# Optimization experiments

Hardware: AMD Instinct MI355X
Metric: run time of the kernel (lower is better)

The kernel has to match this reference:

```python
import jax, jax.numpy as jnp
import numpy as np

NEG_SLOPE = 0.2


def _gat_conv(x, src, dst, W, a_l, a_r, b, n_nodes, activate):
    """DGL-style GATConv. x:[N,F_in], W:[F_in,H*D], a_l/a_r/b:[H,D]."""
    H, D = a_l.shape
    feat = (x @ W).reshape(n_nodes, H, D)                      # [N,H,D]
    el = jnp.sum(feat * a_l, axis=-1)                          # [N,H]
    er = jnp.sum(feat * a_r, axis=-1)                          # [N,H]
    e = jax.nn.leaky_relu(el[src] + er[dst], NEG_SLOPE)        # [E,H]
    # edge softmax over incoming edges of each dst node (numerically stable)
    emax = jax.ops.segment_max(e, dst, num_segments=n_nodes)   # [N,H]
    emax = jnp.where(jnp.isfinite(emax), emax, 0.0)            # zero-in-degree safe
    ee = jnp.exp(e - emax[dst])                                # [E,H]
    denom = jax.ops.segment_sum(ee, dst, num_segments=n_nodes) # [N,H]
    alpha = ee / jnp.maximum(denom[dst], 1e-9)                 # [E,H]
    # aggregate alpha-weighted src features into dst
    msg = alpha[:, :, None] * feat[src]                        # [E,H,D]
    out = jax.ops.segment_sum(msg, dst, num_segments=n_nodes)  # [N,H,D]
    out = out + b
    if activate:
        out = jax.nn.elu(out)
    return out


def setup_inputs() -> dict:
    key = jax.random.key(0)
    ks = jax.random.split(key, 16)
    N, E, F_in, H, Dh, C = 50000, 800000, 256, 4, 64, 40
    s = lambda fan_in: 1.0 / np.sqrt(fan_in)
    return {
        "x": jax.random.normal(ks[0], (N, F_in), dtype=jnp.float32),
        "edge_index": jax.random.randint(ks[1], (2, E), 0, N, dtype=jnp.int32),
        "W0": jax.random.normal(ks[2], (F_in, H * Dh), dtype=jnp.float32) * s(F_in),
        "al0": jax.random.normal(ks[3], (H, Dh), dtype=jnp.float32) * s(Dh),
        "ar0": jax.random.normal(ks[4], (H, Dh), dtype=jnp.float32) * s(Dh),
        "b0": jnp.zeros((H, Dh), dtype=jnp.float32),
        "W1": jax.random.normal(ks[5], (H * Dh, H * Dh), dtype=jnp.float32) * s(H * Dh),
        "al1": jax.random.normal(ks[6], (H, Dh), dtype=jnp.float32) * s(Dh),
        "ar1": jax.random.normal(ks[7], (H, Dh), dtype=jnp.float32) * s(Dh),
        "b1": jnp.zeros((H, Dh), dtype=jnp.float32),
        "W2": jax.random.normal(ks[8], (H * Dh, H * C), dtype=jnp.float32) * s(H * Dh),
        "al2": jax.random.normal(ks[9], (H, C), dtype=jnp.float32) * s(C),
        "ar2": jax.random.normal(ks[10], (H, C), dtype=jnp.float32) * s(C),
        "b2": jnp.zeros((H, C), dtype=jnp.float32),
    }


def reference(x, edge_index, W0, al0, ar0, b0, W1, al1, ar1, b1, W2, al2, ar2, b2):
    N = x.shape[0]
    src, dst = edge_index[0], edge_index[1]
    h = _gat_conv(x, src, dst, W0, al0, ar0, b0, N, activate=True).reshape(N, -1)
    h = _gat_conv(h, src, dst, W1, al1, ar1, b1, N, activate=True).reshape(N, -1)
    out = _gat_conv(h, src, dst, W2, al2, ar2, b2, N, activate=False)
    logits = out.mean(axis=1)  # mean over heads -> [N, num_classes]
    return logits
```

## Files before the change

### kernel.cpp

```cpp
#include <hip/hip_runtime.h>
#include <hip/hip_bf16.h>
#include <math.h>

#define NEG_SLOPE 0.2f

typedef unsigned short ushortT;
typedef __attribute__((ext_vector_type(8))) short short8;
typedef __attribute__((ext_vector_type(4))) float f32x4;

static __device__ __forceinline__ float leaky(float x){ return x > 0.f ? x : NEG_SLOPE * x; }
static __device__ __forceinline__ float elu(float x){ return x > 0.f ? x : (__expf(x) - 1.f); }

static __device__ __forceinline__ ushortT f2bf(float f){
  unsigned u = __float_as_uint(f);
  u += 0x7fff + ((u >> 16) & 1);
  return (ushortT)(u >> 16);
}
static __device__ __forceinline__ float bf2f(ushortT h){ return __uint_as_float((unsigned)h << 16); }
static __device__ __forceinline__ float bf_lo(unsigned u){ return __uint_as_float(u << 16); }
static __device__ __forceinline__ float bf_hi(unsigned u){ return __uint_as_float(u & 0xffff0000u); }

__global__ void hist_kernel(const int* __restrict__ dst, int E, int* __restrict__ counts){
  int i = blockIdx.x*blockDim.x + threadIdx.x;
  if(i < E) atomicAdd(&counts[dst[i]], 1);
}

__global__ void scan1_kernel(const int* __restrict__ counts, int N,
                             int* __restrict__ offsets, int* __restrict__ blocksums){
  __shared__ int sdata[1024];
  int i = blockIdx.x*1024 + threadIdx.x;
  int v = (i<N) ? counts[i] : 0;
  sdata[threadIdx.x] = v;
  __syncthreads();
  for(int off=1; off<1024; off<<=1){
    int t = (threadIdx.x >= off) ? sdata[threadIdx.x-off] : 0;
    __syncthreads();
    sdata[threadIdx.x] += t;
    __syncthreads();
  }
  if(i<N) offsets[i] = sdata[threadIdx.x] - v;
  if(threadIdx.x==1023) blocksums[blockIdx.x] = sdata[1023];
}

__global__ void scan2_kernel(int* __restrict__ blocksums, int nb){
  __shared__ int sdata[64];
  int v = ((int)threadIdx.x < nb) ? blocksums[threadIdx.x] : 0;
  sdata[threadIdx.x] = v;
  __syncthreads();
  for(int off=1; off<64; off<<=1){
    int t = (threadIdx.x >= off) ? sdata[threadIdx.x-off] : 0;
    __syncthreads();
    sdata[threadIdx.x] += t;
    __syncthreads();
  }
  if((int)threadIdx.x < nb) blocksums[threadIdx.x] = sdata[threadIdx.x] - v;
}

__global__ void scan3_kernel(int* __restrict__ offsets, const int* __restrict__ blocksums,
                             int N, int E, int* __restrict__ cursor){
  int i = blockIdx.x*1024 + threadIdx.x;
  if(i < N){
    int o = offsets[i] + blocksums[blockIdx.x];
    offsets[i] = o;
    cursor[i] = o;
  }
  if(i == 0) offsets[N] = E;
}

__global__ void scatter_kernel(const int* __restrict__ src, const int* __restrict__ dst, int E,
                               int* __restrict__ cursor, int* __restrict__ ssrc,
                               int* __restrict__ sdst){
  int i = blockIdx.x*blockDim.x + threadIdx.x;
  if(i < E){
    int d = dst[i];
    int p = atomicAdd(&cursor[d], 1);
    ssrc[p] = src[i];
    sdst[p] = d;
  }
}

__global__ __launch_bounds__(256) void wsplit_kernel(const float* __restrict__ W, int N,
                              ushortT* __restrict__ Wth, ushortT* __restrict__ Wtl){
  int idx = blockIdx.x*256 + threadIdx.x;
  int n = idx >> 8, k = idx & 255;
  float v = (n < N) ? W[(size_t)k*N + n] : 0.f;
  ushortT h = f2bf(v);
  ushortT l = f2bf(v - bf2f(h));
  Wth[idx] = h; Wtl[idx] = l;
}

#define GBM 128
#define GBN 128
#define GBK 32
#define LSTR 40
__global__ __launch_bounds__(256) void gemm_mfma(const float* __restrict__ A,
                       const ushortT* __restrict__ Bth, const ushortT* __restrict__ Btl,
                       ushortT* __restrict__ Cm, int M, int N, int K){
  __shared__ ushortT Ah[GBM*LSTR], Al[GBM*LSTR], Bh[GBN*LSTR], Bl[GBN*LSTR];
  const int tid  = threadIdx.x;
  const int lane = tid & 63;
  const int wv   = tid >> 6;
  const int wr   = wv >> 1, wc = wv & 1;
  const int m0   = blockIdx.y * GBM;
  const int n0   = blockIdx.x * GBN;
  const int l15  = lane & 15, quad = lane >> 4;

  f32x4 acc[4][4];
  #pragma unroll
  for(int i=0;i<4;i++)
    #pragma unroll
    for(int j=0;j<4;j++){ acc[i][j][0]=0.f; acc[i][j][1]=0.f; acc[i][j][2]=0.f; acc[i][j][3]=0.f; }

  for(int k0=0; k0<K; k0+=GBK){
    #pragma unroll
    for(int i=0;i<4;i++){
      int r  = (tid>>3) + i*32;
      int cq = (tid&7)*4;
      float4 v = make_float4(0.f,0.f,0.f,0.f);
      int gm = m0 + r;
      if(gm < M) v = *(const float4*)&A[(size_t)gm*K + k0 + cq];
      ushortT h0=f2bf(v.x), h1=f2bf(v.y), h2=f2bf(v.z), h3=f2bf(v.w);
      ushort4 hv = make_ushort4(h0,h1,h2,h3);
      ushort4 lv = make_ushort4(f2bf(v.x-bf2f(h0)), f2bf(v.y-bf2f(h1)),
                                f2bf(v.z-bf2f(h2)), f2bf(v.w-bf2f(h3)));
      *(ushort4*)&Ah[r*LSTR + cq] = hv;
      *(ushort4*)&Al[r*LSTR + cq] = lv;
    }
    {
      int n  = tid >> 1;
      int kh = (tid & 1) * 16;
      const ushortT* bhrow = &Bth[(size_t)(n0+n)*K + k0 + kh];
      const ushortT* blrow = &Btl[(size_t)(n0+n)*K + k0 + kh];
      uint4 hv0 = *(const uint4*)(bhrow);
      uint4 hv1 = *(const uint4*)(bhrow + 8);
      uint4 lv0 = *(const uint4*)(blrow);
      uint4 lv1 = *(const uint4*)(blrow + 8);
      *(uint4*)&Bh[n*LSTR + kh]     = hv0;
      *(uint4*)&Bh[n*LSTR + kh + 8] = hv1;
      *(uint4*)&Bl[n*LSTR + kh]     = lv0;
      *(uint4*)&Bl[n*LSTR + kh + 8] = lv1;
    }
    __syncthreads();
    short8 a_h[4], a_l[4], b_h[4], b_l[4];
    #pragma unroll
    for(int i=0;i<4;i++){
      int m = wr*64 + i*16 + l15;
      a_h[i] = *(short8*)&Ah[m*LSTR + quad*8];
      a_l[i] = *(short8*)&Al[m*LSTR + quad*8];
    }
    #pragma unroll
    for(int j=0;j<4;j++){
      int n = wc*64 + j*16 + l15;
      b_h[j] = *(short8*)&Bh[n*LSTR + quad*8];
      b_l[j] = *(short8*)&Bl[n*LSTR + quad*8];
    }
    #pragma unroll
    for(int i=0;i<4;i++)
      #pragma unroll
      for(int j=0;j<4;j++){
        acc[i][j] = __builtin_amdgcn_mfma_f32_16x16x32_bf16(a_h[i], b_h[j], acc[i][j], 0,0,0);
        acc[i][j] = __builtin_amdgcn_mfma_f32_16x16x32_bf16(a_h[i], b_l[j], acc[i][j], 0,0,0);
        acc[i][j] = __builtin_amdgcn_mfma_f32_16x16x32_bf16(a_l[i], b_h[j], acc[i][j], 0,0,0);
      }
    __syncthreads();
  }
  #pragma unroll
  for(int i=0;i<4;i++){
    #pragma unroll
    for(int r=0;r<4;r++){
      int gm = m0 + wr*64 + i*16 + quad*4 + r;
      if(gm >= M) continue;
      #pragma unroll
      for(int j=0;j<4;j++){
        int gn = n0 + wc*64 + j*16 + l15;
        if(gn < N) Cm[(size_t)gm*N + gn] = f2bf(acc[i][j][r]);
      }
    }
  }
}

__global__ void attn_proj_bf(const __hip_bfloat16* __restrict__ feat, const float* __restrict__ a_l,
                             const float* __restrict__ a_r, float* __restrict__ el,
                             float* __restrict__ er, int D){
  int n = blockIdx.x;
  int h = threadIdx.x >> 6;
  int lane = threadIdx.x & 63;
  float vl = 0.f, vr = 0.f;
  for(int d=lane; d<D; d+=64){
    float f = (float)feat[(size_t)n*4*D + h*D + d];
    vl = fmaf(f, a_l[h*D+d], vl);
    vr = fmaf(f, a_r[h*D+d], vr);
  }
  #pragma unroll
  for(int off=32; off; off>>=1){ vl += __shfl_down(vl,off); vr += __shfl_down(vr,off); }
  if(lane==0){ el[n*4+h] = vl; er[n*4+h] = vr; }
}

__global__ __launch_bounds__(256) void edge_w_kernel(const int* __restrict__ ssrc,
                              const int* __restrict__ sdst, int E,
                              const float4* __restrict__ el4, const float4* __restrict__ er4,
                              float4* __restrict__ ew){
  int e = blockIdx.x*blockDim.x + threadIdx.x;
  if(e >= E) return;
  int s = ssrc[e], d = sdst[e];
  float4 l = el4[s], r = er4[d];
  float4 w;
  w.x = __expf(leaky(l.x + r.x));
  w.y = __expf(leaky(l.y + r.y));
  w.z = __expf(leaky(l.z + r.z));
  w.w = __expf(leaky(l.w + r.w));
  ew[e] = w;
}

__global__ __launch_bounds__(256) void agg_kernel(const uint2* __restrict__ feat2,
                           const float* __restrict__ ew,
                           const int* __restrict__ offsets, const int* __restrict__ ssrc,
                           const float* __restrict__ bias, float* __restrict__ outp, int N){
  int wv = threadIdx.x >> 6;
  int lane = threadIdx.x & 63;
  int n = blockIdx.x*4 + wv;
  if(n >= N) return;
  int h = lane >> 4;
  int e0 = offsets[n], e1 = offsets[n+1];
  float4 acc0 = make_float4(0.f,0.f,0.f,0.f), acc1 = acc0, acc2 = acc0, acc3 = acc0;
  float den0 = 0.f, den1 = 0.f, den2 = 0.f, den3 = 0.f;
  int e = e0;
  for(; e+3 < e1; e += 4){
    int s0 = ssrc[e], s1 = ssrc[e+1], s2 = ssrc[e+2], s3 = ssrc[e+3];
    float w0 = ew[(size_t)e*4 + h];
    float w1 = ew[(size_t)(e+1)*4 + h];
    float w2 = ew[(size_t)(e+2)*4 + h];
    float w3 = ew[(size_t)(e+3)*4 + h];
    uint2 q0 = feat2[(size_t)s0*64 + lane];
    uint2 q1 = feat2[(size_t)s1*64 + lane];
    uint2 q2 = feat2[(size_t)s2*64 + lane];
    uint2 q3 = feat2[(size_t)s3*64 + lane];
    acc0.x = fmaf(w0,bf_lo(q0.x),acc0.x); acc0.y = fmaf(w0,bf_hi(q0.x),acc0.y);
    acc0.z = fmaf(w0,bf_lo(q0.y),acc0.z); acc0.w = fmaf(w0,bf_hi(q0.y),acc0.w); den0 += w0;
    acc1.x = fmaf(w1,bf_lo(q1.x),acc1.x); acc1.y = fmaf(w1,bf_hi(q1.x),acc1.y);
    acc1.z = fmaf(w1,bf_lo(q1.y),acc1.z); acc1.w = fmaf(w1,bf_hi(q1.y),acc1.w); den1 += w1;
    acc2.x = fmaf(w2,bf_lo(q2.x),acc2.x); acc2.y = fmaf(w2,bf_hi(q2.x),acc2.y);
    acc2.z = fmaf(w2,bf_lo(q2.y),acc2.z); acc2.w = fmaf(w2,bf_hi(q2.y),acc2.w); den2 += w2;
    acc3.x = fmaf(w3,bf_lo(q3.x),acc3.x); acc3.y = fmaf(w3,bf_hi(q3.x),acc3.y);
    acc3.z = fmaf(w3,bf_lo(q3.y),acc3.z); acc3.w = fmaf(w3,bf_hi(q3.y),acc3.w); den3 += w3;
  }
  for(; e < e1; e++){
    int s = ssrc[e];
    float w = ew[(size_t)e*4 + h];
    uint2 q = feat2[(size_t)s*64 + lane];
    acc0.x = fmaf(w,bf_lo(q.x),acc0.x); acc0.y = fmaf(w,bf_hi(q.x),acc0.y);
    acc0.z = fmaf(w,bf_lo(q.y),acc0.z); acc0.w = fmaf(w,bf_hi(q.y),acc0.w); den0 += w;
  }
  float denom = (den0+den1) + (den2+den3);
  float4 acc;
  acc.x = (acc0.x+acc1.x) + (acc2.x+acc3.x);
  acc.y = (acc0.y+acc1.y) + (acc2.y+acc3.y);
  acc.z = (acc0.z+acc1.z) + (acc2.z+acc3.z);
  acc.w = (acc0.w+acc1.w) + (acc2.w+acc3.w);
  float inv = 1.f / fmaxf(denom, 1e-9f);
  float4 b4 = *(const float4*)&bias[lane*4];
  float4 o;
  o.x = elu(acc.x*inv + b4.x);
  o.y = elu(acc.y*inv + b4.y);
  o.z = elu(acc.z*inv + b4.z);
  o.w = elu(acc.w*inv + b4.w);
  *(float4*)&outp[(size_t)n*256 + lane*4] = o;
}

__global__ __launch_bounds__(256) void agg2_kernel(const uint2* __restrict__ feat2,
                            const float* __restrict__ ew,
                            const int* __restrict__ offsets, const int* __restrict__ ssrc,
                            const float* __restrict__ bias, float* __restrict__ logits, int N){
  __shared__ float s_out[4][160];
  int wv = threadIdx.x >> 6;
  int lane = threadIdx.x & 63;
  int n = blockIdx.x*4 + wv;
  bool valid = (n < N);
  if(valid && lane < 40){
    int h = lane / 10;
    int e0 = offsets[n], e1 = offsets[n+1];
    float4 acc0 = make_float4(0.f,0.f,0.f,0.f), acc1 = acc0, acc2 = acc0, acc3 = acc0;
    float den0 = 0.f, den1 = 0.f, den2 = 0.f, den3 = 0.f;
    int e = e0;
    for(; e+3 < e1; e += 4){
      int s0 = ssrc[e], s1 = ssrc[e+1], s2 = ssrc[e+2], s3 = ssrc[e+3];
      float w0 = ew[(size_t)e*4 + h];
      float w1 = ew[(size_t)(e+1)*4 + h];
      float w2 = ew[(size_t)(e+2)*4 + h];
      float w3 = ew[(size_t)(e+3)*4 + h];
      uint2 q0 = feat2[(size_t)s0*40 + lane];
      uint2 q1 = feat2[(size_t)s1*40 + lane];
      uint2 q2 = feat2[(size_t)s2*40 + lane];
      uint2 q3 = feat2[(size_t)s3*40 + lane];
      acc0.x = fmaf(w0,bf_lo(q0.x),acc0.x); acc0.y = fmaf(w0,bf_hi(q0.x),acc0.y);
      acc0.z = fmaf(w0,bf_lo(q0.y),acc0.z); acc0.w = fmaf(w0,bf_hi(q0.y),acc0.w); den0 += w0;
      acc1.x = fmaf(w1,bf_lo(q1.x),acc1.x); acc1.y = fmaf(w1,bf_hi(q1.x),acc1.y);
      acc1.z = fmaf(w1,bf_lo(q1.y),acc1.z); acc1.w = fmaf(w1,bf_hi(q1.y),acc1.w); den1 += w1;
      acc2.x = fmaf(w2,bf_lo(q2.x),acc2.x); acc2.y = fmaf(w2,bf_hi(q2.x),acc2.y);
      acc2.z = fmaf(w2,bf_lo(q2.y),acc2.z); acc2.w = fmaf(w2,bf_hi(q2.y),acc2.w); den2 += w2;
      acc3.x = fmaf(w3,bf_lo(q3.x),acc3.x); acc3.y = fmaf(w3,bf_hi(q3.x),acc3.y);
      acc3.z = fmaf(w3,bf_lo(q3.y),acc3.z); acc3.w = fmaf(w3,bf_hi(q3.y),acc3.w); den3 += w3;
    }
    for(; e < e1; e++){
      int s = ssrc[e];
      float w = ew[(size_t)e*4 + h];
      uint2 q = feat2[(size_t)s*40 + lane];
      acc0.x = fmaf(w,bf_lo(q.x),acc0.x); acc0.y = fmaf(w,bf_hi(q.x),acc0.y);
      acc0.z = fmaf(w,bf_lo(q.y),acc0.z); acc0.w = fmaf(w,bf_hi(q.y),acc0.w); den0 += w;
    }
    float denom = (den0+den1) + (den2+den3);
    float4 acc;
    acc.x = (acc0.x+acc1.x) + (acc2.x+acc3.x);
    acc.y = (acc0.y+acc1.y) + (acc2.y+acc3.y);
    acc.z = (acc0.z+acc1.z) + (acc2.z+acc3.z);
    acc.w = (acc0.w+acc1.w) + (acc2.w+acc3.w);
    float inv = 1.f / fmaxf(denom, 1e-9f);
    float4 b4 = *(const float4*)&bias[lane*4];
    s_out[wv][lane*4+0] = acc.x*inv + b4.x;
    s_out[wv][lane*4+1] = acc.y*inv + b4.y;
    s_out[wv][lane*4+2] = acc.z*inv + b4.z;
    s_out[wv][lane*4+3] = acc.w*inv + b4.w;
  }
  __syncthreads();
  if(valid && lane < 40){
    logits[(size_t)n*40 + lane] =
        0.25f * (s_out[wv][lane] + s_out[wv][40+lane] + s_out[wv][80+lane] + s_out[wv][120+lane]);
  }
}

extern "C" void kernel_launch(void* const* d_in, const int* in_sizes, int n_in,
                              void* d_out, int out_size, void* d_ws, size_t ws_size,
                              hipStream_t stream){
  const float* x   = (const float*)d_in[0];
  const int*   eix = (const int*)  d_in[1];
  const float* W0  = (const float*)d_in[2];
  const float* al0 = (const float*)d_in[3];
  const float* ar0 = (const float*)d_in[4];
  const float* b0  = (const float*)d_in[5];
  const float* W1  = (const float*)d_in[6];
  const float* al1 = (const float*)d_in[7];
  const float* ar1 = (const float*)d_in[8];
  const float* b1  = (const float*)d_in[9];
  const float* W2  = (const float*)d_in[10];
  const float* al2 = (const float*)d_in[11];
  const float* ar2 = (const float*)d_in[12];
  const float* b2  = (const float*)d_in[13];
  float* logits = (float*)d_out;

  const int N = in_sizes[0] / 256;
  const int E = in_sizes[1] / 2;
  const int* src = eix;
  const int* dst = eix + E;
  const int nb = (N + 1023) / 1024;

  char* ws = (char*)d_ws;
  auto alloc = [&](size_t bytes)->char*{
    char* p = ws; ws += (bytes + 255) & ~(size_t)255; return p;
  };
  int*   counts    = (int*)  alloc((size_t)N*4);
  int*   offsets   = (int*)  alloc((size_t)(N+1)*4);
  int*   cursor    = (int*)  alloc((size_t)N*4);
  int*   blocksums = (int*)  alloc((size_t)nb*4);
  int*   ssrc      = (int*)  alloc((size_t)E*4);
  int*   sdst      = (int*)  alloc((size_t)E*4);
  float* ew        = (float*)alloc((size_t)E*4*4);
  __hip_bfloat16* bufF = (__hip_bfloat16*)alloc((size_t)N*256*2);
  float* bufH      = (float*)alloc((size_t)N*256*4);
  float* el_buf    = (float*)alloc((size_t)N*4*4);
  float* er_buf    = (float*)alloc((size_t)N*4*4);
  ushortT* Wth0 = (ushortT*)alloc(256*256*2);
  ushortT* Wtl0 = (ushortT*)alloc(256*256*2);
  ushortT* Wth1 = (ushortT*)alloc(256*256*2);
  ushortT* Wtl1 = (ushortT*)alloc(256*256*2);
  ushortT* Wth2 = (ushortT*)alloc(256*256*2);
  ushortT* Wtl2 = (ushortT*)alloc(256*256*2);

  hipMemsetAsync(counts, 0, (size_t)N*4, stream);
  hist_kernel   <<<(E+255)/256, 256, 0, stream>>>(dst, E, counts);
  scan1_kernel  <<<nb, 1024, 0, stream>>>(counts, N, offsets, blocksums);
  scan2_kernel  <<<1, 64, 0, stream>>>(blocksums, nb);
  scan3_kernel  <<<nb, 1024, 0, stream>>>(offsets, blocksums, N, E, cursor);
  scatter_kernel<<<(E+255)/256, 256, 0, stream>>>(src, dst, E, cursor, ssrc, sdst);

  wsplit_kernel<<<256, 256, 0, stream>>>(W0, 256, Wth0, Wtl0);
  wsplit_kernel<<<256, 256, 0, stream>>>(W1, 256, Wth1, Wtl1);
  wsplit_kernel<<<256, 256, 0, stream>>>(W2, 160, Wth2, Wtl2);

  dim3 gg(2, (N + GBM - 1)/GBM);
  int aggGrid = (N+3)/4;
  int ewGrid  = (E+255)/256;
  gemm_mfma<<<gg, 256, 0, stream>>>(x, Wth0, Wtl0, (ushortT*)bufF, N, 256, 256);
  attn_proj_bf<<<N, 256, 0, stream>>>(bufF, al0, ar0, el_buf, er_buf, 64);
  edge_w_kernel<<<ewGrid, 256, 0, stream>>>(ssrc, sdst, E, (const float4*)el_buf, (const float4*)er_buf, (float4*)ew);
  agg_kernel<<<aggGrid, 256, 0, stream>>>((const uint2*)bufF, ew, offsets, ssrc, b0, bufH, N);
  gemm_mfma<<<gg, 256, 0, stream>>>(bufH, Wth1, Wtl1, (ushortT*)bufF, N, 256, 256);
  attn_proj_bf<<<N, 256, 0, stream>>>(bufF, al1, ar1, el_buf, er_buf, 64);
  edge_w_kernel<<<ewGrid, 256, 0, stream>>>(ssrc, sdst, E, (const float4*)el_buf, (const float4*)er_buf, (float4*)ew);
  agg_kernel<<<aggGrid, 256, 0, stream>>>((const uint2*)bufF, ew, offsets, ssrc, b1, bufH, N);
  gemm_mfma<<<gg, 256, 0, stream>>>(bufH, Wth2, Wtl2, (ushortT*)bufF, N, 160, 256);
  attn_proj_bf<<<N, 256, 0, stream>>>(bufF, al2, ar2, el_buf, er_buf, 40);
  edge_w_kernel<<<ewGrid, 256, 0, stream>>>(ssrc, sdst, E, (const float4*)el_buf, (const float4*)er_buf, (float4*)ew);
  agg2_kernel<<<aggGrid, 256, 0, stream>>>((const uint2*)bufF, ew, offsets, ssrc, b2, logits, N);
}
```

Measured before the change: 636.3 us.

## Pre-split activations into bf16 hi/lo and use LDS-free direct-load MFMA GEMM

```diff
diff --git a/kernel.cpp b/kernel.cpp
--- a/kernel.cpp
+++ b/kernel.cpp
@@ -89,90 +89,75 @@
   Wth[idx] = h; Wtl[idx] = l;
 }
 
-#define GBM 128
-#define GBN 128
-#define GBK 32
-#define LSTR 40
-__global__ __launch_bounds__(256) void gemm_mfma(const float* __restrict__ A,
+__global__ __launch_bounds__(256) void xsplit_kernel(const float4* __restrict__ x4,
+                              ushortT* __restrict__ Xh, ushortT* __restrict__ Xl, int total4){
+  int i = blockIdx.x*256 + threadIdx.x;
+  if(i >= total4) return;
+  float4 v = x4[i];
+  ushortT h0=f2bf(v.x), h1=f2bf(v.y), h2=f2bf(v.z), h3=f2bf(v.w);
+  ushort4 hv = make_ushort4(h0,h1,h2,h3);
+  ushort4 lv = make_ushort4(f2bf(v.x-bf2f(h0)), f2bf(v.y-bf2f(h1)),
+                            f2bf(v.z-bf2f(h2)), f2bf(v.w-bf2f(h3)));
+  *(ushort4*)&Xh[(size_t)i*4] = hv;
+  *(ushort4*)&Xl[(size_t)i*4] = lv;
+}
+
+__global__ __launch_bounds__(256, 2) void gemm_direct(const ushortT* __restrict__ Ah,
+                       const ushortT* __restrict__ Al,
                        const ushortT* __restrict__ Bth, const ushortT* __restrict__ Btl,
-                       ushortT* __restrict__ Cm, int M, int N, int K){
-  __shared__ ushortT Ah[GBM*LSTR], Al[GBM*LSTR], Bh[GBN*LSTR], Bl[GBN*LSTR];
-  const int tid  = threadIdx.x;
-  const int lane = tid & 63;
-  const int wv   = tid >> 6;
-  const int wr   = wv >> 1, wc = wv & 1;
-  const int m0   = blockIdx.y * GBM;
-  const int n0   = blockIdx.x * GBN;
+                       ushortT* __restrict__ Cm, int M, int N){
+  const int lane = threadIdx.x & 63;
+  const int wv   = threadIdx.x >> 6;
   const int l15  = lane & 15, quad = lane >> 4;
-
-  f32x4 acc[4][4];
+  const int m0   = (blockIdx.y*4 + wv) * 64;
+  const int n0   = blockIdx.x * 128;
+
+  f32x4 acc[4][8];
   #pragma unroll
   for(int i=0;i<4;i++)
     #pragma unroll
-    for(int j=0;j<4;j++){ acc[i][j][0]=0.f; acc[i][j][1]=0.f; acc[i][j][2]=0.f; acc[i][j][3]=0.f; }
-
-  for(int k0=0; k0<K; k0+=GBK){
+    for(int j=0;j<8;j++){ acc[i][j][0]=0.f; acc[i][j][1]=0.f; acc[i][j][2]=0.f; acc[i][j][3]=0.f; }
+
+  size_t arow[4];
+  #pragma unroll
+  for(int i=0;i<4;i++){
+    int m = m0 + i*16 + l15;
+    arow[i] = (size_t)(m < M ? m : M-1) * 256;
+  }
+  size_t brow[8];
+  #pragma unroll
+  for(int j=0;j<8;j++) brow[j] = (size_t)(n0 + j*16 + l15) * 256;
+
+  #pragma unroll
+  for(int t=0; t<8; t++){
+    const int ko = t*32 + quad*8;
+    short8 a_h[4], a_l[4];
     #pragma unroll
     for(int i=0;i<4;i++){
-      int r  = (tid>>3) + i*32;
-      int cq = (tid&7)*4;
-      float4 v = make_float4(0.f,0.f,0.f,0.f);
-      int gm = m0 + r;
-      if(gm < M) v = *(const float4*)&A[(size_t)gm*K + k0 + cq];
-      ushortT h0=f2bf(v.x), h1=f2bf(v.y), h2=f2bf(v.z), h3=f2bf(v.w);
-      ushort4 hv = make_ushort4(h0,h1,h2,h3);
-      ushort4 lv = make_ushort4(f2bf(v.x-bf2f(h0)), f2bf(v.y-bf2f(h1)),
-                                f2bf(v.z-bf2f(h2)), f2bf(v.w-bf2f(h3)));
-      *(ushort4*)&Ah[r*LSTR + cq] = hv;
-      *(ushort4*)&Al[r*LSTR + cq] = lv;
-    }
-    {
-      int n  = tid >> 1;
-      int kh = (tid & 1) * 16;
-      const ushortT* bhrow = &Bth[(size_t)(n0+n)*K + k0 + kh];
-      const ushortT* blrow = &Btl[(size_t)(n0+n)*K + k0 + kh];
-      uint4 hv0 = *(const uint4*)(bhrow);
-      uint4 hv1 = *(const uint4*)(bhrow + 8);
-      uint4 lv0 = *(const uint4*)(blrow);
-      uint4 lv1 = *(const uint4*)(blrow + 8);
-      *(uint4*)&Bh[n*LSTR + kh]     = hv0;
-      *(uint4*)&Bh[n*LSTR + kh + 8] = hv1;
-      *(uint4*)&Bl[n*LSTR + kh]     = lv0;
-      *(uint4*)&Bl[n*LSTR + kh + 8] = lv1;
-    }
-    __syncthreads();
-    short8 a_h[4], a_l[4], b_h[4], b_l[4];
+      a_h[i] = *(const short8*)&Ah[arow[i] + ko];
+      a_l[i] = *(const short8*)&Al[arow[i] + ko];
+    }
     #pragma unroll
-    for(int i=0;i<4;i++){
-      int m = wr*64 + i*16 + l15;
-      a_h[i] = *(short8*)&Ah[m*LSTR + quad*8];
-      a_l[i] = *(short8*)&Al[m*LSTR + quad*8];
-    }
-    #pragma unroll
-    for(int j=0;j<4;j++){
-      int n = wc*64 + j*16 + l15;
-      b_h[j] = *(short8*)&Bh[n*LSTR + quad*8];
-      b_l[j] = *(short8*)&Bl[n*LSTR + quad*8];
-    }
-    #pragma unroll
-    for(int i=0;i<4;i++)
+    for(int j=0;j<8;j++){
+      short8 b_h = *(const short8*)&Bth[brow[j] + ko];
+      short8 b_l = *(const short8*)&Btl[brow[j] + ko];
       #pragma unroll
-      for(int j=0;j<4;j++){
-        acc[i][j] = __builtin_amdgcn_mfma_f32_16x16x32_bf16(a_h[i], b_h[j], acc[i][j], 0,0,0);
-        acc[i][j] = __builtin_amdgcn_mfma_f32_16x16x32_bf16(a_h[i], b_l[j], acc[i][j], 0,0,0);
-        acc[i][j] = __builtin_amdgcn_mfma_f32_16x16x32_bf16(a_l[i], b_h[j], acc[i][j], 0,0,0);
+      for(int i=0;i<4;i++){
+        acc[i][j] = __builtin_amdgcn_mfma_f32_16x16x32_bf16(a_h[i], b_h, acc[i][j], 0,0,0);
+        acc[i][j] = __builtin_amdgcn_mfma_f32_16x16x32_bf16(a_h[i], b_l, acc[i][j], 0,0,0);
+        acc[i][j] = __builtin_amdgcn_mfma_f32_16x16x32_bf16(a_l[i], b_h, acc[i][j], 0,0,0);
       }
-    __syncthreads();
+    }
   }
   #pragma unroll
   for(int i=0;i<4;i++){
     #pragma unroll
     for(int r=0;r<4;r++){
-      int gm = m0 + wr*64 + i*16 + quad*4 + r;
+      int gm = m0 + i*16 + quad*4 + r;
       if(gm >= M) continue;
       #pragma unroll
-      for(int j=0;j<4;j++){
-        int gn = n0 + wc*64 + j*16 + l15;
+      for(int j=0;j<8;j++){
+        int gn = n0 + j*16 + l15;
         if(gn < N) Cm[(size_t)gm*N + gn] = f2bf(acc[i][j][r]);
       }
     }
@@ -215,7 +200,8 @@
 __global__ __launch_bounds__(256) void agg_kernel(const uint2* __restrict__ feat2,
                            const float* __restrict__ ew,
                            const int* __restrict__ offsets, const int* __restrict__ ssrc,
-                           const float* __restrict__ bias, float* __restrict__ outp, int N){
+                           const float* __restrict__ bias,
+                           ushortT* __restrict__ Hh, ushortT* __restrict__ Hl, int N){
   int wv = threadIdx.x >> 6;
   int lane = threadIdx.x & 63;
   int n = blockIdx.x*4 + wv;
@@ -259,12 +245,16 @@
   acc.w = (acc0.w+acc1.w) + (acc2.w+acc3.w);
   float inv = 1.f / fmaxf(denom, 1e-9f);
   float4 b4 = *(const float4*)&bias[lane*4];
-  float4 o;
-  o.x = elu(acc.x*inv + b4.x);
-  o.y = elu(acc.y*inv + b4.y);
-  o.z = elu(acc.z*inv + b4.z);
-  o.w = elu(acc.w*inv + b4.w);
-  *(float4*)&outp[(size_t)n*256 + lane*4] = o;
+  float o0 = elu(acc.x*inv + b4.x);
+  float o1 = elu(acc.y*inv + b4.y);
+  float o2 = elu(acc.z*inv + b4.z);
+  float o3 = elu(acc.w*inv + b4.w);
+  ushortT h0=f2bf(o0), h1=f2bf(o1), h2=f2bf(o2), h3=f2bf(o3);
+  ushort4 hv = make_ushort4(h0,h1,h2,h3);
+  ushort4 lv = make_ushort4(f2bf(o0-bf2f(h0)), f2bf(o1-bf2f(h1)),
+                            f2bf(o2-bf2f(h2)), f2bf(o3-bf2f(h3)));
+  *(ushort4*)&Hh[(size_t)n*256 + lane*4] = hv;
+  *(ushort4*)&Hl[(size_t)n*256 + lane*4] = lv;
 }
 
 __global__ __launch_bounds__(256) void agg2_kernel(const uint2* __restrict__ feat2,
@@ -365,7 +355,8 @@
   int*   sdst      = (int*)  alloc((size_t)E*4);
   float* ew        = (float*)alloc((size_t)E*4*4);
   __hip_bfloat16* bufF = (__hip_bfloat16*)alloc((size_t)N*256*2);
-  float* bufH      = (float*)alloc((size_t)N*256*4);
+  ushortT* Hh      = (ushortT*)alloc((size_t)N*256*2);
+  ushortT* Hl      = (ushortT*)alloc((size_t)N*256*2);
   float* el_buf    = (float*)alloc((size_t)N*4*4);
   float* er_buf    = (float*)alloc((size_t)N*4*4);
   ushortT* Wth0 = (ushortT*)alloc(256*256*2);
@@ -385,19 +376,21 @@
   wsplit_kernel<<<256, 256, 0, stream>>>(W0, 256, Wth0, Wtl0);
   wsplit_kernel<<<256, 256, 0, stream>>>(W1, 256, Wth1, Wtl1);
   wsplit_kernel<<<256, 256, 0, stream>>>(W2, 160, Wth2, Wtl2);
-
-  dim3 gg(2, (N + GBM - 1)/GBM);
+  int total4 = N*64;
+  xsplit_kernel<<<(total4+255)/256, 256, 0, stream>>>((const float4*)x, Hh, Hl, total4);
+
+  dim3 gg(2, (N + 255)/256);
   int aggGrid = (N+3)/4;
   int ewGrid  = (E+255)/256;
-  gemm_mfma<<<gg, 256, 0, stream>>>(x, Wth0, Wtl0, (ushortT*)bufF, N, 256, 256);
+  gemm_direct<<<gg, 256, 0, stream>>>(Hh, Hl, Wth0, Wtl0, (ushortT*)bufF, N, 256);
   attn_proj_bf<<<N, 256, 0, stream>>>(bufF, al0, ar0, el_buf, er_buf, 64);
   edge_w_kernel<<<ewGrid, 256, 0, stream>>>(ssrc, sdst, E, (const float4*)el_buf, (const float4*)er_buf, (float4*)ew);
-  agg_kernel<<<aggGrid, 256, 0, stream>>>((const uint2*)bufF, ew, offsets, ssrc, b0, bufH, N);
-  gemm_mfma<<<gg, 256, 0, stream>>>(bufH, Wth1, Wtl1, (ushortT*)bufF, N, 256, 256);
+  agg_kernel<<<aggGrid, 256, 0, stream>>>((const uint2*)bufF, ew, offsets, ssrc, b0, Hh, Hl, N);
+  gemm_direct<<<gg, 256, 0, stream>>>(Hh, Hl, Wth1, Wtl1, (ushortT*)bufF, N, 256);
   attn_proj_bf<<<N, 256, 0, stream>>>(bufF, al1, ar1, el_buf, er_buf, 64);
   edge_w_kernel<<<ewGrid, 256, 0, stream>>>(ssrc, sdst, E, (const float4*)el_buf, (const float4*)er_buf, (float4*)ew);
-  agg_kernel<<<aggGrid, 256, 0, stream>>>((const uint2*)bufF, ew, offsets, ssrc, b1, bufH, N);
-  gemm_mfma<<<gg, 256, 0, stream>>>(bufH, Wth2, Wtl2, (ushortT*)bufF, N, 160, 256);
+  agg_kernel<<<aggGrid, 256, 0, stream>>>((const uint2*)bufF, ew, offsets, ssrc, b1, Hh, Hl, N);
+  gemm_direct<<<gg, 256, 0, stream>>>(Hh, Hl, Wth2, Wtl2, (ushortT*)bufF, N, 160);
   attn_proj_bf<<<N, 256, 0, stream>>>(bufF, al2, ar2, el_buf, er_buf, 40);
   edge_w_kernel<<<ewGrid, 256, 0, stream>>>(ssrc, sdst, E, (const float4*)el_buf, (const float4*)er_buf, (float4*)ew);
   agg2_kernel<<<aggGrid, 256, 0, stream>>>((const uint2*)bufF, ew, offsets, ssrc, b2, logits, N);
```

Result: slower. 660.0 us (+3.7%).
